# Optimization experiments

Measured on AMD Instinct MI355X. Metric: run time of the kernel, lower is better.

## Reference

```python
import jax, jax.numpy as jnp
import numpy as np

N = 6144        # total nodes
N_USER = 4096   # main nodes used by fusion head
R = 2           # nb_node_kinds (relations)
K = 3           # attention heads
F_IN = 25       # n_units[0]
F_OUT = 64      # n_units[1]
D2 = 64
NB_CLASSES = 2


def setup_inputs() -> dict:
    key = jax.random.key(0)
    ks = jax.random.split(key, 12)
    # boolean dense adjacency per relation, with guaranteed self-loops so no
    # softmax row is all -inf
    adj = jax.random.uniform(ks[0], (R, N, N)) < 0.01
    eye = jnp.eye(N, dtype=bool)
    hadj = adj | eye[None]
    h = jax.random.normal(ks[1], (N, F_IN), dtype=jnp.float32)
    s = 0.1
    return {
        "hadj": hadj,
        "h": h,
        # per-relation GAT params (xavier-ish scale)
        "w": jax.random.normal(ks[2], (R, K, F_IN, F_OUT), dtype=jnp.float32) * s,
        "a_src": jax.random.normal(ks[3], (R, K, F_OUT, 1), dtype=jnp.float32) * s,
        "a_dst": jax.random.normal(ks[4], (R, K, F_OUT, 1), dtype=jnp.float32) * s,
        "bias": jnp.zeros((R, F_OUT), dtype=jnp.float32),
        # additive attention (store Linear weights as (in, out))
        "aw1": jax.random.normal(ks[5], (F_IN, D2), dtype=jnp.float32) * s,
        "aw2": jax.random.normal(ks[6], (F_OUT, D2), dtype=jnp.float32) * s,
        "am": jax.random.normal(ks[7], (D2, 1), dtype=jnp.float32) * s,
        # fusion fc: in = F_OUT * (R + 1)
        "fc_w": jax.random.normal(ks[8], (F_OUT * (R + 1), NB_CLASSES), dtype=jnp.float32) * s,
        "fc_b": jnp.zeros((NB_CLASSES,), dtype=jnp.float32),
    }


def _gat(x, adj, W, asrc, adst, b):
    # x: (N, f_in), adj: (N, N) bool, W: (K, f_in, f_out)
    hp = jnp.einsum('nf,kfo->kno', x, W)                 # (K, N, f_out)
    s = jnp.einsum('kno,koj->kn', hp, asrc)              # (K, N)
    d = jnp.einsum('kno,koj->kn', hp, adst)              # (K, N)
    attn = s[:, :, None] + d[:, None, :]                 # (K, N, N)
    attn = jax.nn.leaky_relu(attn, negative_slope=0.2)
    attn = jnp.where(adj[None], attn, -jnp.inf)
    attn = jax.nn.softmax(attn, axis=-1)                 # dropout = identity (eval)
    out = jnp.einsum('knm,kmo->kno', attn, hp) + b[None, None, :]
    return out.mean(axis=0)                              # mean over heads -> (N, f_out)


def reference(hadj, h, w, a_src, a_dst, bias, aw1, aw2, am, fc_w, fc_b):
    # per-relation dense GAT (single layer; final layer -> mean over heads)
    embs = [_gat(h, hadj[r], w[r], a_src[r], a_dst[r], bias[r]) for r in range(R)]
    type_aware = jnp.stack([e[:N_USER] for e in embs], axis=1)   # (n_user, R, f_out)
    # additive attention fusion
    feat = h[:N_USER]                                            # (n_user, f_in)
    q = jnp.tanh(
        (feat @ aw1)[:, None, :] + jnp.einsum('nrf,fd->nrd', type_aware, aw2)
    )                                                            # (n_user, R, d2)
    beta = jax.nn.softmax(jnp.einsum('nrd,dj->nr', q, am), axis=-1)
    fusion = jnp.einsum('nr,nrf->nf', beta, type_aware)          # (n_user, f_out)
    cat = jnp.concatenate([type_aware.reshape(N_USER, -1), fusion], axis=-1)
    logits = cat @ fc_w + fc_b                                   # (n_user, nb_classes)
    return jax.nn.log_softmax(logits, axis=-1)
```

## Files before the change

### kernel.cpp

```cpp
#include <hip/hip_runtime.h>
#include <stdint.h>

#define NN 6144
#define NUSER 4096
#define RR 2
#define KK 3
#define FIN 25
#define FOUT 64
#define DD2 64
#define CAP 192

typedef int int4v __attribute__((ext_vector_type(4)));

__device__ __forceinline__ float wave_reduce_sum(float v) {
    #pragma unroll
    for (int off = 32; off >= 1; off >>= 1) v += __shfl_xor(v, off);
    return v;
}
__device__ __forceinline__ unsigned short f2bf(float x) {
    unsigned int u = __float_as_uint(x);
    unsigned int r = (u + 0x7fffu + ((u >> 16) & 1u)) >> 16;
    return (unsigned short)r;
}
__device__ __forceinline__ float bf2f(unsigned short b) {
    return __uint_as_float(((unsigned int)b) << 16);
}

__global__ __launch_bounds__(256) void k1_proj(
    const float* __restrict__ h, const float* __restrict__ w,
    const float* __restrict__ asrc, const float* __restrict__ adst,
    ushort4* __restrict__ hpq, float4* __restrict__ sq, float4* __restrict__ dq)
{
    const int wid  = threadIdx.x >> 6;
    const int lane = threadIdx.x & 63;
    const int row  = blockIdx.x * 4 + wid;
    const int r    = row / NN;
    const int n    = row % NN;

    const float* hrow = h + (size_t)n * FIN;
    float acc[KK];
    #pragma unroll
    for (int k = 0; k < KK; ++k) {
        const float* wp = w + ((size_t)(r * KK + k) * FIN) * FOUT + lane;
        float a = 0.f;
        #pragma unroll
        for (int f = 0; f < FIN; ++f) a += hrow[f] * wp[f * FOUT];
        acc[k] = a;
    }

    ushort4 pk;
    pk.x = f2bf(acc[0]); pk.y = f2bf(acc[1]); pk.z = f2bf(acc[2]); pk.w = 0;
    hpq[(size_t)row * FOUT + lane] = pk;

    float sv0 = wave_reduce_sum(acc[0] * asrc[(r * KK + 0) * FOUT + lane]);
    float sv1 = wave_reduce_sum(acc[1] * asrc[(r * KK + 1) * FOUT + lane]);
    float sv2 = wave_reduce_sum(acc[2] * asrc[(r * KK + 2) * FOUT + lane]);
    float dv0 = wave_reduce_sum(acc[0] * adst[(r * KK + 0) * FOUT + lane]);
    float dv1 = wave_reduce_sum(acc[1] * adst[(r * KK + 1) * FOUT + lane]);
    float dv2 = wave_reduce_sum(acc[2] * adst[(r * KK + 2) * FOUT + lane]);
    if (lane == 0) {
        sq[row] = make_float4(sv0, sv1, sv2, 0.f);
        dq[row] = make_float4(dv0, dv1, dv2, 0.f);
    }
}

__global__ __launch_bounds__(256) void kSG(
    const int* __restrict__ hadj, const ushort4* __restrict__ hpq,
    const float4* __restrict__ sq, const float4* __restrict__ dq,
    const float* __restrict__ bias, float* __restrict__ embs)
{
    const int wid  = threadIdx.x >> 6;
    const int lane = threadIdx.x & 63;
    const int urow = blockIdx.x * 4 + wid;
    const int r    = urow / NUSER;
    const int n    = urow - r * NUSER;

    __shared__ int   nbr_s[4][CAP];
    __shared__ float pw_s[4][3][CAP];
    int* nbr = nbr_s[wid];
    float (*pw)[CAP] = pw_s[wid];

    const int* rowp = hadj + ((size_t)r * NN + n) * NN;
    const unsigned long long below = (1ull << lane) - 1ull;
    int base = 0;
    #pragma unroll 8
    for (int t = 0; t < 24; ++t) {
        const int m0 = t * 256 + lane * 4;
        const int4v v = *reinterpret_cast<const int4v*>(rowp + m0);
        const unsigned long long b0 = __ballot(v.x != 0);
        const unsigned long long b1 = __ballot(v.y != 0);
        const unsigned long long b2 = __ballot(v.z != 0);
        const unsigned long long b3 = __ballot(v.w != 0);
        const int n0 = __popcll(b0), n1 = __popcll(b1);
        const int n2 = __popcll(b2), n3 = __popcll(b3);
        const int o0 = base + __popcll(b0 & below);
        const int o1 = base + n0 + __popcll(b1 & below);
        const int o2 = base + n0 + n1 + __popcll(b2 & below);
        const int o3 = base + n0 + n1 + n2 + __popcll(b3 & below);
        if (v.x && o0 < CAP) nbr[o0] = m0 + 0;
        if (v.y && o1 < CAP) nbr[o1] = m0 + 1;
        if (v.z && o2 < CAP) nbr[o2] = m0 + 2;
        if (v.w && o3 < CAP) nbr[o3] = m0 + 3;
        base += n0 + n1 + n2 + n3;
    }
    const int count = base > CAP ? CAP : base;

    const float4 sv = sq[(size_t)r * NN + n];
    const float4* dqr = dq + (size_t)r * NN;
    float ss0 = 0.f, ss1 = 0.f, ss2 = 0.f;
    for (int j = lane; j < count; j += 64) {
        const float4 dv = dqr[nbr[j]];
        float e0 = sv.x + dv.x; e0 = (e0 >= 0.f) ? e0 : 0.2f * e0;
        float e1 = sv.y + dv.y; e1 = (e1 >= 0.f) ? e1 : 0.2f * e1;
        float e2 = sv.z + dv.z; e2 = (e2 >= 0.f) ? e2 : 0.2f * e2;
        float p0 = __expf(e0); pw[0][j] = p0; ss0 += p0;
        float p1 = __expf(e1); pw[1][j] = p1; ss1 += p1;
        float p2 = __expf(e2); pw[2][j] = p2; ss2 += p2;
    }
    ss0 = wave_reduce_sum(ss0);
    ss1 = wave_reduce_sum(ss1);
    ss2 = wave_reduce_sum(ss2);

    const ushort4* hq = hpq + ((size_t)r * NN) * FOUT + lane;
    float a0 = 0.f, a1 = 0.f, a2 = 0.f;
    int j = 0;
    for (; j + 4 <= count; j += 4) {
        #pragma unroll
        for (int u = 0; u < 4; ++u) {
            const ushort4 v = hq[(size_t)nbr[j + u] * FOUT];
            a0 += pw[0][j + u] * bf2f(v.x);
            a1 += pw[1][j + u] * bf2f(v.y);
            a2 += pw[2][j + u] * bf2f(v.z);
        }
    }
    for (; j < count; ++j) {
        const ushort4 v = hq[(size_t)nbr[j] * FOUT];
        a0 += pw[0][j] * bf2f(v.x);
        a1 += pw[1][j] * bf2f(v.y);
        a2 += pw[2][j] * bf2f(v.z);
    }

    const float tot = a0 / ss0 + a1 / ss1 + a2 / ss2;
    embs[(size_t)urow * FOUT + lane] = tot * (1.f / 3.f) + bias[r * FOUT + lane];
}

__global__ __launch_bounds__(64) void k3_fuse(
    const float* __restrict__ h, const float* __restrict__ embs,
    const float* __restrict__ aw1, const float* __restrict__ aw2,
    const float* __restrict__ am, const float* __restrict__ fcw,
    const float* __restrict__ fcb, float* __restrict__ out)
{
    const int n = blockIdx.x;
    const int o = threadIdx.x;

    __shared__ float sh[2][FOUT];
    const float ta0 = embs[((size_t)0 * NUSER + n) * FOUT + o];
    const float ta1 = embs[((size_t)1 * NUSER + n) * FOUT + o];
    sh[0][o] = ta0;
    sh[1][o] = ta1;

    float fa = 0.f;
    const float* hrow = h + (size_t)n * FIN;
    #pragma unroll
    for (int f = 0; f < FIN; ++f) fa += hrow[f] * aw1[f * DD2 + o];
    __syncthreads();

    float e[2];
    #pragma unroll
    for (int r = 0; r < 2; ++r) {
        float t = fa;
        #pragma unroll 8
        for (int jj = 0; jj < FOUT; ++jj) t += sh[r][jj] * aw2[jj * DD2 + o];
        float q = tanhf(t);
        e[r] = wave_reduce_sum(q * am[o]);
    }
    const float mx = fmaxf(e[0], e[1]);
    float b0 = __expf(e[0] - mx), b1 = __expf(e[1] - mx);
    const float inv = 1.f / (b0 + b1);
    b0 *= inv; b1 *= inv;
    const float fus = b0 * ta0 + b1 * ta1;

    float p0 = ta0 * fcw[(o      ) * 2 + 0] + ta1 * fcw[(64 + o) * 2 + 0] + fus * fcw[(128 + o) * 2 + 0];
    float p1 = ta0 * fcw[(o      ) * 2 + 1] + ta1 * fcw[(64 + o) * 2 + 1] + fus * fcw[(128 + o) * 2 + 1];
    const float lg0 = wave_reduce_sum(p0) + fcb[0];
    const float lg1 = wave_reduce_sum(p1) + fcb[1];

    if (o == 0) {
        const float m2  = fmaxf(lg0, lg1);
        const float lse = m2 + logf(__expf(lg0 - m2) + __expf(lg1 - m2));
        out[(size_t)n * 2 + 0] = lg0 - lse;
        out[(size_t)n * 2 + 1] = lg1 - lse;
    }
}

extern "C" void kernel_launch(void* const* d_in, const int* in_sizes, int n_in,
                              void* d_out, int out_size, void* d_ws, size_t ws_size,
                              hipStream_t stream)
{
    const int*   hadj = (const int*)d_in[0];
    const float* h    = (const float*)d_in[1];
    const float* w    = (const float*)d_in[2];
    const float* asrc = (const float*)d_in[3];
    const float* adst = (const float*)d_in[4];
    const float* bias = (const float*)d_in[5];
    const float* aw1  = (const float*)d_in[6];
    const float* aw2  = (const float*)d_in[7];
    const float* am   = (const float*)d_in[8];
    const float* fcw  = (const float*)d_in[9];
    const float* fcb  = (const float*)d_in[10];
    float* out = (float*)d_out;

    char* ws = (char*)d_ws;
    ushort4* hpq = (ushort4*)ws;
    ws += (size_t)RR * NN * FOUT * sizeof(ushort4);
    float4* sq = (float4*)ws;
    ws += (size_t)RR * NN * sizeof(float4);
    float4* dq = (float4*)ws;
    ws += (size_t)RR * NN * sizeof(float4);
    float* embs = (float*)ws;

    k1_proj<<<RR * NN / 4,    256, 0, stream>>>(h, w, asrc, adst, hpq, sq, dq);
    kSG    <<<RR * NUSER / 4, 256, 0, stream>>>(hadj, hpq, sq, dq, bias, embs);
    k3_fuse<<<NUSER, 64, 0, stream>>>(h, embs, aw1, aw2, am, fcw, fcb, out);
}
```

Measured before the change: 80.55 us.

## Fuse fusion head into sparse GAT kernel with multi-row waves

Merges the attention-fusion/classifier kernel into the GAT aggregation kernel. Each wave now processes four rows (both relations for two user nodes) and keeps the embeddings in shared memory, removing the global embs round-trip and one launch. The gather loop is also unrolled by 8. In exchange, the grid shrinks to 512 blocks of serialized per-wave work, which reduces parallelism and the latency hiding on the dominant adjacency-scan memory traffic.

```diff
diff --git a/kernel.cpp b/kernel.cpp
--- a/kernel.cpp
+++ b/kernel.cpp
@@ -9,6 +9,9 @@
 #define FOUT 64
 #define DD2 64
 #define CAP 192
+
+#define NWAVE 2048
+#define ROWS_PER_WAVE 4
 
 typedef int int4v __attribute__((ext_vector_type(4)));
 
@@ -67,129 +70,131 @@
 __global__ __launch_bounds__(256) void kSG(
     const int* __restrict__ hadj, const ushort4* __restrict__ hpq,
     const float4* __restrict__ sq, const float4* __restrict__ dq,
-    const float* __restrict__ bias, float* __restrict__ embs)
-{
-    const int wid  = threadIdx.x >> 6;
-    const int lane = threadIdx.x & 63;
-    const int urow = blockIdx.x * 4 + wid;
-    const int r    = urow / NUSER;
-    const int n    = urow - r * NUSER;
-
-    __shared__ int   nbr_s[4][CAP];
-    __shared__ float pw_s[4][3][CAP];
-    int* nbr = nbr_s[wid];
-    float (*pw)[CAP] = pw_s[wid];
-
-    const int* rowp = hadj + ((size_t)r * NN + n) * NN;
-    const unsigned long long below = (1ull << lane) - 1ull;
-    int base = 0;
-    #pragma unroll 8
-    for (int t = 0; t < 24; ++t) {
-        const int m0 = t * 256 + lane * 4;
-        const int4v v = *reinterpret_cast<const int4v*>(rowp + m0);
-        const unsigned long long b0 = __ballot(v.x != 0);
-        const unsigned long long b1 = __ballot(v.y != 0);
-        const unsigned long long b2 = __ballot(v.z != 0);
-        const unsigned long long b3 = __ballot(v.w != 0);
-        const int n0 = __popcll(b0), n1 = __popcll(b1);
-        const int n2 = __popcll(b2), n3 = __popcll(b3);
-        const int o0 = base + __popcll(b0 & below);
-        const int o1 = base + n0 + __popcll(b1 & below);
-        const int o2 = base + n0 + n1 + __popcll(b2 & below);
-        const int o3 = base + n0 + n1 + n2 + __popcll(b3 & below);
-        if (v.x && o0 < CAP) nbr[o0] = m0 + 0;
-        if (v.y && o1 < CAP) nbr[o1] = m0 + 1;
-        if (v.z && o2 < CAP) nbr[o2] = m0 + 2;
-        if (v.w && o3 < CAP) nbr[o3] = m0 + 3;
-        base += n0 + n1 + n2 + n3;
-    }
-    const int count = base > CAP ? CAP : base;
-
-    const float4 sv = sq[(size_t)r * NN + n];
-    const float4* dqr = dq + (size_t)r * NN;
-    float ss0 = 0.f, ss1 = 0.f, ss2 = 0.f;
-    for (int j = lane; j < count; j += 64) {
-        const float4 dv = dqr[nbr[j]];
-        float e0 = sv.x + dv.x; e0 = (e0 >= 0.f) ? e0 : 0.2f * e0;
-        float e1 = sv.y + dv.y; e1 = (e1 >= 0.f) ? e1 : 0.2f * e1;
-        float e2 = sv.z + dv.z; e2 = (e2 >= 0.f) ? e2 : 0.2f * e2;
-        float p0 = __expf(e0); pw[0][j] = p0; ss0 += p0;
-        float p1 = __expf(e1); pw[1][j] = p1; ss1 += p1;
-        float p2 = __expf(e2); pw[2][j] = p2; ss2 += p2;
-    }
-    ss0 = wave_reduce_sum(ss0);
-    ss1 = wave_reduce_sum(ss1);
-    ss2 = wave_reduce_sum(ss2);
-
-    const ushort4* hq = hpq + ((size_t)r * NN) * FOUT + lane;
-    float a0 = 0.f, a1 = 0.f, a2 = 0.f;
-    int j = 0;
-    for (; j + 4 <= count; j += 4) {
-        #pragma unroll
-        for (int u = 0; u < 4; ++u) {
-            const ushort4 v = hq[(size_t)nbr[j + u] * FOUT];
-            a0 += pw[0][j + u] * bf2f(v.x);
-            a1 += pw[1][j + u] * bf2f(v.y);
-            a2 += pw[2][j + u] * bf2f(v.z);
-        }
-    }
-    for (; j < count; ++j) {
-        const ushort4 v = hq[(size_t)nbr[j] * FOUT];
-        a0 += pw[0][j] * bf2f(v.x);
-        a1 += pw[1][j] * bf2f(v.y);
-        a2 += pw[2][j] * bf2f(v.z);
-    }
-
-    const float tot = a0 / ss0 + a1 / ss1 + a2 / ss2;
-    embs[(size_t)urow * FOUT + lane] = tot * (1.f / 3.f) + bias[r * FOUT + lane];
-}
-
-__global__ __launch_bounds__(64) void k3_fuse(
-    const float* __restrict__ h, const float* __restrict__ embs,
+    const float* __restrict__ bias, const float* __restrict__ h,
     const float* __restrict__ aw1, const float* __restrict__ aw2,
     const float* __restrict__ am, const float* __restrict__ fcw,
     const float* __restrict__ fcb, float* __restrict__ out)
 {
-    const int n = blockIdx.x;
-    const int o = threadIdx.x;
-
-    __shared__ float sh[2][FOUT];
-    const float ta0 = embs[((size_t)0 * NUSER + n) * FOUT + o];
-    const float ta1 = embs[((size_t)1 * NUSER + n) * FOUT + o];
-    sh[0][o] = ta0;
-    sh[1][o] = ta1;
-
-    float fa = 0.f;
-    const float* hrow = h + (size_t)n * FIN;
+    const int wid  = threadIdx.x >> 6;
+    const int lane = threadIdx.x & 63;
+    const int g    = blockIdx.x * 4 + wid;
+
+    __shared__ int   nbr_s[4][CAP];
+    __shared__ float pw_s[4][3][CAP];
+    __shared__ float emb_sh[4][ROWS_PER_WAVE][FOUT];
+    int* nbr = nbr_s[wid];
+    float (*pw)[CAP] = pw_s[wid];
+
+    const unsigned long long below = (1ull << lane) - 1ull;
+
+    #pragma unroll 1
+    for (int rr = 0; rr < ROWS_PER_WAVE; ++rr) {
+        const int urow = g + rr * NWAVE;
+        const int r    = urow >> 12;
+        const int n    = urow & 4095;
+
+        const int* rowp = hadj + ((size_t)r * NN + n) * NN;
+        int base = 0;
+        #pragma unroll 8
+        for (int t = 0; t < 24; ++t) {
+            const int m0 = t * 256 + lane * 4;
+            const int4v v = *reinterpret_cast<const int4v*>(rowp + m0);
+            const unsigned long long b0 = __ballot(v.x != 0);
+            const unsigned long long b1 = __ballot(v.y != 0);
+            const unsigned long long b2 = __ballot(v.z != 0);
+            const unsigned long long b3 = __ballot(v.w != 0);
+            const int n0 = __popcll(b0), n1 = __popcll(b1);
+            const int n2 = __popcll(b2), n3 = __popcll(b3);
+            const int o0 = base + __popcll(b0 & below);
+            const int o1 = base + n0 + __popcll(b1 & below);
+            const int o2 = base + n0 + n1 + __popcll(b2 & below);
+            const int o3 = base + n0 + n1 + n2 + __popcll(b3 & below);
+            if (v.x && o0 < CAP) nbr[o0] = m0 + 0;
+            if (v.y && o1 < CAP) nbr[o1] = m0 + 1;
+            if (v.z && o2 < CAP) nbr[o2] = m0 + 2;
+            if (v.w && o3 < CAP) nbr[o3] = m0 + 3;
+            base += n0 + n1 + n2 + n3;
+        }
+        const int count = base > CAP ? CAP : base;
+
+        const float4 sv = sq[(size_t)r * NN + n];
+        const float4* dqr = dq + (size_t)r * NN;
+        float ss0 = 0.f, ss1 = 0.f, ss2 = 0.f;
+        for (int j = lane; j < count; j += 64) {
+            const float4 dv = dqr[nbr[j]];
+            float e0 = sv.x + dv.x; e0 = (e0 >= 0.f) ? e0 : 0.2f * e0;
+            float e1 = sv.y + dv.y; e1 = (e1 >= 0.f) ? e1 : 0.2f * e1;
+            float e2 = sv.z + dv.z; e2 = (e2 >= 0.f) ? e2 : 0.2f * e2;
+            float p0 = __expf(e0); pw[0][j] = p0; ss0 += p0;
+            float p1 = __expf(e1); pw[1][j] = p1; ss1 += p1;
+            float p2 = __expf(e2); pw[2][j] = p2; ss2 += p2;
+        }
+        ss0 = wave_reduce_sum(ss0);
+        ss1 = wave_reduce_sum(ss1);
+        ss2 = wave_reduce_sum(ss2);
+
+        const ushort4* hq = hpq + ((size_t)r * NN) * FOUT + lane;
+        float a0 = 0.f, a1 = 0.f, a2 = 0.f;
+        int j = 0;
+        for (; j + 8 <= count; j += 8) {
+            #pragma unroll
+            for (int u = 0; u < 8; ++u) {
+                const ushort4 v = hq[(size_t)nbr[j + u] * FOUT];
+                a0 += pw[0][j + u] * bf2f(v.x);
+                a1 += pw[1][j + u] * bf2f(v.y);
+                a2 += pw[2][j + u] * bf2f(v.z);
+            }
+        }
+        for (; j < count; ++j) {
+            const ushort4 v = hq[(size_t)nbr[j] * FOUT];
+            a0 += pw[0][j] * bf2f(v.x);
+            a1 += pw[1][j] * bf2f(v.y);
+            a2 += pw[2][j] * bf2f(v.z);
+        }
+
+        emb_sh[wid][rr][lane] = (a0 / ss0 + a1 / ss1 + a2 / ss2) * (1.f / 3.f)
+                              + bias[r * FOUT + lane];
+    }
+
+    const int o = lane;
     #pragma unroll
-    for (int f = 0; f < FIN; ++f) fa += hrow[f] * aw1[f * DD2 + o];
-    __syncthreads();
-
-    float e[2];
-    #pragma unroll
-    for (int r = 0; r < 2; ++r) {
-        float t = fa;
-        #pragma unroll 8
-        for (int jj = 0; jj < FOUT; ++jj) t += sh[r][jj] * aw2[jj * DD2 + o];
-        float q = tanhf(t);
-        e[r] = wave_reduce_sum(q * am[o]);
-    }
-    const float mx = fmaxf(e[0], e[1]);
-    float b0 = __expf(e[0] - mx), b1 = __expf(e[1] - mx);
-    const float inv = 1.f / (b0 + b1);
-    b0 *= inv; b1 *= inv;
-    const float fus = b0 * ta0 + b1 * ta1;
-
-    float p0 = ta0 * fcw[(o      ) * 2 + 0] + ta1 * fcw[(64 + o) * 2 + 0] + fus * fcw[(128 + o) * 2 + 0];
-    float p1 = ta0 * fcw[(o      ) * 2 + 1] + ta1 * fcw[(64 + o) * 2 + 1] + fus * fcw[(128 + o) * 2 + 1];
-    const float lg0 = wave_reduce_sum(p0) + fcb[0];
-    const float lg1 = wave_reduce_sum(p1) + fcb[1];
-
-    if (o == 0) {
-        const float m2  = fmaxf(lg0, lg1);
-        const float lse = m2 + logf(__expf(lg0 - m2) + __expf(lg1 - m2));
-        out[(size_t)n * 2 + 0] = lg0 - lse;
-        out[(size_t)n * 2 + 1] = lg1 - lse;
+    for (int a = 0; a < 2; ++a) {
+        const int n = g + a * NWAVE;
+        const float ta0 = emb_sh[wid][a][o];
+        const float ta1 = emb_sh[wid][a + 2][o];
+
+        float fa = 0.f;
+        const float* hrow = h + (size_t)n * FIN;
+        #pragma unroll
+        for (int f = 0; f < FIN; ++f) fa += hrow[f] * aw1[f * DD2 + o];
+
+        float e[2];
+        #pragma unroll
+        for (int q = 0; q < 2; ++q) {
+            float t = fa;
+            const float* es = emb_sh[wid][a + 2 * q];
+            #pragma unroll 8
+            for (int jj = 0; jj < FOUT; ++jj) t += es[jj] * aw2[jj * DD2 + o];
+            float qq = tanhf(t);
+            e[q] = wave_reduce_sum(qq * am[o]);
+        }
+        const float mxe = fmaxf(e[0], e[1]);
+        float b0 = __expf(e[0] - mxe), b1 = __expf(e[1] - mxe);
+        const float inv = 1.f / (b0 + b1);
+        b0 *= inv; b1 *= inv;
+        const float fus = b0 * ta0 + b1 * ta1;
+
+        float p0 = ta0 * fcw[(o      ) * 2 + 0] + ta1 * fcw[(64 + o) * 2 + 0] + fus * fcw[(128 + o) * 2 + 0];
+        float p1 = ta0 * fcw[(o      ) * 2 + 1] + ta1 * fcw[(64 + o) * 2 + 1] + fus * fcw[(128 + o) * 2 + 1];
+        const float lg0 = wave_reduce_sum(p0) + fcb[0];
+        const float lg1 = wave_reduce_sum(p1) + fcb[1];
+
+        if (o == 0) {
+            const float m2  = fmaxf(lg0, lg1);
+            const float lse = m2 + logf(__expf(lg0 - m2) + __expf(lg1 - m2));
+            out[(size_t)n * 2 + 0] = lg0 - lse;
+            out[(size_t)n * 2 + 1] = lg1 - lse;
+        }
     }
 }
 
@@ -216,10 +221,8 @@
     float4* sq = (float4*)ws;
     ws += (size_t)RR * NN * sizeof(float4);
     float4* dq = (float4*)ws;
-    ws += (size_t)RR * NN * sizeof(float4);
-    float* embs = (float*)ws;
-
-    k1_proj<<<RR * NN / 4,    256, 0, stream>>>(h, w, asrc, adst, hpq, sq, dq);
-    kSG    <<<RR * NUSER / 4, 256, 0, stream>>>(hadj, hpq, sq, dq, bias, embs);
-    k3_fuse<<<NUSER, 64, 0, stream>>>(h, embs, aw1, aw2, am, fcw, fcb, out);
-}
+
+    k1_proj<<<RR * NN / 4, 256, 0, stream>>>(h, w, asrc, adst, hpq, sq, dq);
+    kSG<<<NWAVE / 4, 256, 0, stream>>>(
+        hadj, hpq, sq, dq, bias, h, aw1, aw2, am, fcw, fcb, out);
+}
```

Result: slower. 107.4 us (+33.3%).
